# Optimization experiments

Hardware: AMD Instinct MI355X
Metric: run time of the kernel (lower is better)

## Reference

```python
import jax, jax.numpy as jnp
import numpy as np

HEAD_DIM = 4  # hard-coded by rosa_4bit_layer's reshape(B, T, -1, 4)


def setup_inputs() -> dict:
    key = jax.random.key(0)
    B, T, C = 4, 4096, 512
    kq, kk, kv = jax.random.split(key, 3)
    xq = jax.random.normal(kq, (B, T, C), dtype=jnp.float32)
    xk = jax.random.normal(kk, (B, T, C), dtype=jnp.float32)
    xv = jax.random.normal(kv, (B, T, C), dtype=jnp.float32)
    emb = jnp.ones((1, 1, C), dtype=jnp.float32)  # nn.Parameter(torch.ones((1,1,C)))
    return {"xq": xq, "xk": xk, "xv": xv, "emb": emb}


def _rosa_sufa(q, k, v):
    # q,k,v: (B, H, T, d) with d = 4.
    # Causal linear-attention recurrence with per-head d x d state:
    #   S_t = S_{t-1} + k_t v_t^T ;  o_t = q_t^T S_t
    # expressed as a cumulative sum over outer products (vectorized over T).
    kv = jnp.cumsum(k[..., :, None] * v[..., None, :], axis=2)  # (B,H,T,d,d)
    return jnp.einsum('bhtd,bhtde->bhte', q, kv)                # (B,H,T,d)


def reference(xq, xk, xv, emb):
    B, T, C = xq.shape
    H = C // HEAD_DIM
    # (B,T,C) -> (B,T,H,4) -> (B,H,T,4)
    q = xq.reshape(B, T, H, HEAD_DIM).transpose(0, 2, 1, 3)
    k = xk.reshape(B, T, H, HEAD_DIM).transpose(0, 2, 1, 3)
    v = xv.reshape(B, T, H, HEAD_DIM).transpose(0, 2, 1, 3)
    o = _rosa_sufa(q, k, v)
    # (B,H,T,4) -> (B,T,C)
    o = o.transpose(0, 2, 1, 3).reshape(B, T, C)
    return o * emb
```

## Files before the change

### kernel.cpp

```cpp
#include <hip/hip_runtime.h>


constexpr int B   = 4;
constexpr int T   = 4096;
constexpr int C   = 512;
constexpr int CT  = 32;
constexpr int NC  = T / CT;
constexpr int SC  = 16;
constexpr int NSC = NC / SC;
constexpr size_t SPART_OFF = (size_t)B * NC * 2048;

__global__ __launch_bounds__(512) void rosa_partial(const float* __restrict__ k,
                                                    const float* __restrict__ v,
                                                    float* __restrict__ part) {
  const int bc  = blockIdx.x;
  const int b   = bc / NC;
  const int c   = bc % NC;
  const int tid = threadIdx.x;
  const int h   = tid >> 2;
  const int e   = tid & 3;

  const size_t base = ((size_t)b * T + (size_t)c * CT) * (size_t)C + (h << 2);
  const float* kb = k + base;
  const float* vb = v + base + e;

  float4 acc = {0.f, 0.f, 0.f, 0.f};
#pragma unroll 8
  for (int t = 0; t < CT; ++t) {
    const float4 k4 = *reinterpret_cast<const float4*>(kb + (size_t)t * C);
    const float  ve = vb[(size_t)t * C];
    acc.x += k4.x * ve;
    acc.y += k4.y * ve;
    acc.z += k4.z * ve;
    acc.w += k4.w * ve;
  }
  reinterpret_cast<float4*>(part)[(size_t)bc * 512 + tid] = acc;
}

__global__ __launch_bounds__(128) void rosa_super(const float* __restrict__ part,
                                                  float* __restrict__ spart) {
  const int blk = blockIdx.x;
  const int g   = blk & 3;
  const int bs  = blk >> 2;
  const int b   = bs / NSC;
  const int s   = bs % NSC;
  const int j   = (g << 7) + threadIdx.x;

  const float4* p4 = reinterpret_cast<const float4*>(part) +
                     ((size_t)(b * NC + s * SC)) * 512 + j;
  float4 acc = {0.f, 0.f, 0.f, 0.f};
#pragma unroll
  for (int i = 0; i < SC; ++i) {
    const float4 v4 = p4[(size_t)i * 512];
    acc.x += v4.x;
    acc.y += v4.y;
    acc.z += v4.z;
    acc.w += v4.w;
  }
  reinterpret_cast<float4*>(spart)[(size_t)bs * 512 + j] = acc;
}

__global__ __launch_bounds__(512) void rosa_scan_out(const float* __restrict__ q,
                                                     const float* __restrict__ k,
                                                     const float* __restrict__ v,
                                                     const float* __restrict__ emb,
                                                     const float* __restrict__ part,
                                                     const float* __restrict__ spart,
                                                     float* __restrict__ out) {
  const int bc  = blockIdx.x;
  const int b   = bc / NC;
  const int c   = bc % NC;
  const int tid = threadIdx.x;
  const int h   = tid >> 2;
  const int e   = tid & 3;
  const int s   = c >> 4;
  const int cr  = c & (SC - 1);

  float4 S = {0.f, 0.f, 0.f, 0.f};
  const float4* sp = reinterpret_cast<const float4*>(spart) + (size_t)b * NSC * 512 + tid;
#pragma unroll 4
  for (int i = 0; i < s; ++i) {
    const float4 p4 = sp[(size_t)i * 512];
    S.x += p4.x; S.y += p4.y; S.z += p4.z; S.w += p4.w;
  }
  const float4* pb = reinterpret_cast<const float4*>(part) +
                     ((size_t)(b * NC + s * SC)) * 512 + tid;
#pragma unroll 4
  for (int i = 0; i < cr; ++i) {
    const float4 p4 = pb[(size_t)i * 512];
    S.x += p4.x; S.y += p4.y; S.z += p4.z; S.w += p4.w;
  }

  const size_t base = ((size_t)b * T + (size_t)c * CT) * (size_t)C + (h << 2);
  const float* qb = q + base;
  const float* kb = k + base;
  const float* vb = v + base + e;
  float*       ob = out + base + e;
  const float embv = emb[(h << 2) + e];

#pragma unroll 8
  for (int t = 0; t < CT; ++t) {
    const float4 k4 = *reinterpret_cast<const float4*>(kb + (size_t)t * C);
    const float4 q4 = *reinterpret_cast<const float4*>(qb + (size_t)t * C);
    const float  ve = vb[(size_t)t * C];
    S.x += k4.x * ve;
    S.y += k4.y * ve;
    S.z += k4.z * ve;
    S.w += k4.w * ve;
    const float o = q4.x * S.x + q4.y * S.y + q4.z * S.z + q4.w * S.w;
    ob[(size_t)t * C] = o * embv;
  }
}

extern "C" void kernel_launch(void* const* d_in, const int* in_sizes, int n_in,
                              void* d_out, int out_size, void* d_ws, size_t ws_size,
                              hipStream_t stream) {
  const float* xq  = (const float*)d_in[0];
  const float* xk  = (const float*)d_in[1];
  const float* xv  = (const float*)d_in[2];
  const float* emb = (const float*)d_in[3];
  float* out   = (float*)d_out;
  float* part  = (float*)d_ws;
  float* spart = part + SPART_OFF;

  rosa_partial<<<B * NC, 512, 0, stream>>>(xk, xv, part);
  rosa_super<<<B * NSC * 4, 128, 0, stream>>>(part, spart);
  rosa_scan_out<<<B * NC, 512, 0, stream>>>(xq, xk, xv, emb, part, spart, out);
}
```

Baseline: 151.3 us.

## Fuse three scan kernels into one cooperative kernel with grid syncs

Merges the chunk-partial, super-chunk sum and scan/output kernels into a single cooperative launch. Each block handles two chunks and the phases are separated by grid-wide barriers. The aim is to remove two kernel launch gaps and drain points. The cost is two grid syncs, a requirement that all 256 blocks be co-resident, and a fallback to the three-kernel path if the cooperative launch fails.

```diff
diff --git a/kernel.cpp b/kernel.cpp
--- a/kernel.cpp
+++ b/kernel.cpp
@@ -1,4 +1,7 @@
 #include <hip/hip_runtime.h>
+#include <hip/hip_cooperative_groups.h>
+
+namespace cg = cooperative_groups;
 
 
 constexpr int B   = 4;
@@ -8,87 +11,55 @@
 constexpr int NC  = T / CT;
 constexpr int SC  = 16;
 constexpr int NSC = NC / SC;
+constexpr int CPB = 2;
 constexpr size_t SPART_OFF = (size_t)B * NC * 2048;
 
-__global__ __launch_bounds__(512) void rosa_partial(const float* __restrict__ k,
-                                                    const float* __restrict__ v,
-                                                    float* __restrict__ part) {
-  const int bc  = blockIdx.x;
-  const int b   = bc / NC;
-  const int c   = bc % NC;
-  const int tid = threadIdx.x;
-  const int h   = tid >> 2;
-  const int e   = tid & 3;
 
+__device__ __forceinline__ void chunk_partial(const float* __restrict__ k,
+                                              const float* __restrict__ v,
+                                              float* __restrict__ part,
+                                              int bc, int tid) {
+  const int b = bc / NC, c = bc % NC;
+  const int h = tid >> 2, e = tid & 3;
   const size_t base = ((size_t)b * T + (size_t)c * CT) * (size_t)C + (h << 2);
   const float* kb = k + base;
   const float* vb = v + base + e;
-
   float4 acc = {0.f, 0.f, 0.f, 0.f};
 #pragma unroll 8
   for (int t = 0; t < CT; ++t) {
     const float4 k4 = *reinterpret_cast<const float4*>(kb + (size_t)t * C);
     const float  ve = vb[(size_t)t * C];
-    acc.x += k4.x * ve;
-    acc.y += k4.y * ve;
-    acc.z += k4.z * ve;
-    acc.w += k4.w * ve;
+    acc.x += k4.x * ve; acc.y += k4.y * ve;
+    acc.z += k4.z * ve; acc.w += k4.w * ve;
   }
   reinterpret_cast<float4*>(part)[(size_t)bc * 512 + tid] = acc;
 }
 
-__global__ __launch_bounds__(128) void rosa_super(const float* __restrict__ part,
-                                                  float* __restrict__ spart) {
-  const int blk = blockIdx.x;
-  const int g   = blk & 3;
-  const int bs  = blk >> 2;
-  const int b   = bs / NSC;
-  const int s   = bs % NSC;
-  const int j   = (g << 7) + threadIdx.x;
-
-  const float4* p4 = reinterpret_cast<const float4*>(part) +
-                     ((size_t)(b * NC + s * SC)) * 512 + j;
-  float4 acc = {0.f, 0.f, 0.f, 0.f};
-#pragma unroll
-  for (int i = 0; i < SC; ++i) {
-    const float4 v4 = p4[(size_t)i * 512];
-    acc.x += v4.x;
-    acc.y += v4.y;
-    acc.z += v4.z;
-    acc.w += v4.w;
-  }
-  reinterpret_cast<float4*>(spart)[(size_t)bs * 512 + j] = acc;
-}
-
-__global__ __launch_bounds__(512) void rosa_scan_out(const float* __restrict__ q,
-                                                     const float* __restrict__ k,
-                                                     const float* __restrict__ v,
-                                                     const float* __restrict__ emb,
-                                                     const float* __restrict__ part,
-                                                     const float* __restrict__ spart,
-                                                     float* __restrict__ out) {
-  const int bc  = blockIdx.x;
-  const int b   = bc / NC;
-  const int c   = bc % NC;
-  const int tid = threadIdx.x;
-  const int h   = tid >> 2;
-  const int e   = tid & 3;
-  const int s   = c >> 4;
-  const int cr  = c & (SC - 1);
+__device__ __forceinline__ void chunk_scan_out(const float* __restrict__ q,
+                                               const float* __restrict__ k,
+                                               const float* __restrict__ v,
+                                               const float* __restrict__ emb,
+                                               const float* __restrict__ part,
+                                               const float* __restrict__ spart,
+                                               float* __restrict__ out,
+                                               int bc, int tid) {
+  const int b = bc / NC, c = bc % NC;
+  const int h = tid >> 2, e = tid & 3;
+  const int s = c >> 4, cr = c & (SC - 1);
 
   float4 S = {0.f, 0.f, 0.f, 0.f};
   const float4* sp = reinterpret_cast<const float4*>(spart) + (size_t)b * NSC * 512 + tid;
 #pragma unroll 4
   for (int i = 0; i < s; ++i) {
-    const float4 p4 = sp[(size_t)i * 512];
-    S.x += p4.x; S.y += p4.y; S.z += p4.z; S.w += p4.w;
+    const float4 x = sp[(size_t)i * 512];
+    S.x += x.x; S.y += x.y; S.z += x.z; S.w += x.w;
   }
   const float4* pb = reinterpret_cast<const float4*>(part) +
                      ((size_t)(b * NC + s * SC)) * 512 + tid;
 #pragma unroll 4
   for (int i = 0; i < cr; ++i) {
-    const float4 p4 = pb[(size_t)i * 512];
-    S.x += p4.x; S.y += p4.y; S.z += p4.z; S.w += p4.w;
+    const float4 x = pb[(size_t)i * 512];
+    S.x += x.x; S.y += x.y; S.z += x.z; S.w += x.w;
   }
 
   const size_t base = ((size_t)b * T + (size_t)c * CT) * (size_t)C + (h << 2);
@@ -103,13 +74,73 @@
     const float4 k4 = *reinterpret_cast<const float4*>(kb + (size_t)t * C);
     const float4 q4 = *reinterpret_cast<const float4*>(qb + (size_t)t * C);
     const float  ve = vb[(size_t)t * C];
-    S.x += k4.x * ve;
-    S.y += k4.y * ve;
-    S.z += k4.z * ve;
-    S.w += k4.w * ve;
+    S.x += k4.x * ve; S.y += k4.y * ve;
+    S.z += k4.z * ve; S.w += k4.w * ve;
     const float o = q4.x * S.x + q4.y * S.y + q4.z * S.z + q4.w * S.w;
     ob[(size_t)t * C] = o * embv;
   }
+}
+
+__device__ __forceinline__ void super_sum(const float* __restrict__ part,
+                                          float* __restrict__ spart,
+                                          int bs, int tid) {
+  const int sb = bs / NSC, ss = bs % NSC;
+  const float4* p4 = reinterpret_cast<const float4*>(part) +
+                     ((size_t)(sb * NC + ss * SC)) * 512 + tid;
+  float4 sa = {0.f, 0.f, 0.f, 0.f};
+#pragma unroll
+  for (int i = 0; i < SC; ++i) {
+    const float4 x = p4[(size_t)i * 512];
+    sa.x += x.x; sa.y += x.y; sa.z += x.z; sa.w += x.w;
+  }
+  reinterpret_cast<float4*>(spart)[(size_t)bs * 512 + tid] = sa;
+}
+
+
+__global__ __launch_bounds__(512, 4) void rosa_fused(const float* __restrict__ q,
+                                                     const float* __restrict__ k,
+                                                     const float* __restrict__ v,
+                                                     const float* __restrict__ emb,
+                                                     float* __restrict__ part,
+                                                     float* __restrict__ spart,
+                                                     float* __restrict__ out) {
+  const int tid = threadIdx.x;
+#pragma unroll
+  for (int i = 0; i < CPB; ++i)
+    chunk_partial(k, v, part, blockIdx.x * CPB + i, tid);
+
+  cg::this_grid().sync();
+
+  if (blockIdx.x < B * NSC)
+    super_sum(part, spart, blockIdx.x, tid);
+
+  cg::this_grid().sync();
+
+#pragma unroll
+  for (int i = 0; i < CPB; ++i)
+    chunk_scan_out(q, k, v, emb, part, spart, out, blockIdx.x * CPB + i, tid);
+}
+
+
+__global__ __launch_bounds__(512) void rosa_partial(const float* __restrict__ k,
+                                                    const float* __restrict__ v,
+                                                    float* __restrict__ part) {
+  chunk_partial(k, v, part, blockIdx.x, threadIdx.x);
+}
+
+__global__ __launch_bounds__(512) void rosa_super(const float* __restrict__ part,
+                                                  float* __restrict__ spart) {
+  super_sum(part, spart, blockIdx.x, threadIdx.x);
+}
+
+__global__ __launch_bounds__(512) void rosa_scan_out(const float* __restrict__ q,
+                                                     const float* __restrict__ k,
+                                                     const float* __restrict__ v,
+                                                     const float* __restrict__ emb,
+                                                     const float* __restrict__ part,
+                                                     const float* __restrict__ spart,
+                                                     float* __restrict__ out) {
+  chunk_scan_out(q, k, v, emb, part, spart, out, blockIdx.x, threadIdx.x);
 }
 
 extern "C" void kernel_launch(void* const* d_in, const int* in_sizes, int n_in,
@@ -123,7 +154,14 @@
   float* part  = (float*)d_ws;
   float* spart = part + SPART_OFF;
 
-  rosa_partial<<<B * NC, 512, 0, stream>>>(xk, xv, part);
-  rosa_super<<<B * NSC * 4, 128, 0, stream>>>(part, spart);
-  rosa_scan_out<<<B * NC, 512, 0, stream>>>(xq, xk, xv, emb, part, spart, out);
+  void* args[] = {(void*)&xq, (void*)&xk, (void*)&xv, (void*)&emb,
+                  (void*)&part, (void*)&spart, (void*)&out};
+  hipError_t err = hipLaunchCooperativeKernel((const void*)rosa_fused,
+                                              dim3(B * NC / CPB), dim3(512),
+                                              args, 0, stream);
+  if (err != hipSuccess) {
+    rosa_partial<<<B * NC, 512, 0, stream>>>(xk, xv, part);
+    rosa_super<<<B * NSC, 512, 0, stream>>>(part, spart);
+    rosa_scan_out<<<B * NC, 512, 0, stream>>>(xq, xk, xv, emb, part, spart, out);
+  }
 }
```

New measurement: 229.3 us. +51.6%, slower.
